# Kernel tuning notes

Hardware: AMD Instinct MI355X
Metric: run time of the kernel (lower is better)

Reference implementation:

```python
import jax, jax.numpy as jnp
import numpy as np

VOCAB = 50257
H = 512
T = 1024


def setup_inputs() -> dict:
    key = jax.random.key(0)
    k1, k2, k3, k4 = jax.random.split(key, 4)
    return {
        "tokens": jax.random.randint(k1, (T,), 0, VOCAB),
        "h0": jnp.zeros((H,), jnp.float32),
        "input_hidden": jax.random.normal(k2, (VOCAB, H), jnp.float32) * 0.01,
        "hidden_hidden": jax.random.normal(k3, (H, H), jnp.float32) * 0.01,
        "bias_hidden": jnp.zeros((H,), jnp.float32),
        "combined_weight": jax.random.normal(k4, (2 * H, VOCAB), jnp.float32) * 0.01,
        "bias_output": jnp.zeros((VOCAB,), jnp.float32),
    }


def reference(tokens, h0, input_hidden, hidden_hidden, bias_hidden,
              combined_weight, bias_output):
    T_ = tokens.shape[0]
    pos = jnp.arange(T_)
    emb = input_hidden[tokens]  # one-hot @ input_hidden == row gather, [T, H]

    def step(carry, xt):
        h, hist = carry              # h: [H], hist: [T, H] (rows >= t are zero)
        e, t = xt
        h = jnp.tanh(e + h @ hidden_hidden + bias_hidden)          # RNN cell
        scores = hist @ h                                          # [T]
        valid = pos < t                                            # causal mask over cache
        w = jax.nn.softmax(jnp.where(valid, scores, -1e30))
        ctx = jnp.where(t > 0, w @ hist, jnp.zeros_like(h))        # empty cache -> zeros
        out = jnp.concatenate([h, ctx]) @ combined_weight + bias_output
        hist = hist.at[t].set(h)
        return (h, hist), out

    init = (h0, jnp.zeros((T_, h0.shape[0]), h0.dtype))
    _, outs = jax.lax.scan(step, init, (emb, pos))
    return outs  # [T, VOCAB]
```

## Files before the change

kernel.cpp:

```cpp
#include <hip/hip_runtime.h>

typedef __attribute__((ext_vector_type(4))) float f32x4;
typedef __attribute__((ext_vector_type(8))) short short8;
typedef unsigned long long u64;

#define VOCAB 50257
#define HDIM 512
#define TLEN 1024
#define RNN_WGS 16
#define NANBITS 0x7fc00000u

#define GLOBAL_AS __attribute__((address_space(1)))
#define LDS_AS __attribute__((address_space(3)))
#define ASYNC16(gsrc, ldst) \
  __builtin_amdgcn_global_load_lds((const GLOBAL_AS void*)(gsrc), (LDS_AS void*)(ldst), 16, 0, 0)

static __device__ __forceinline__ unsigned short f2bf(float f) {
  unsigned u = __float_as_uint(f);
  u += 0x7fffu + ((u >> 16) & 1u);
  return (unsigned short)(u >> 16);
}
static __device__ __forceinline__ float b2f(short s) {
  return __uint_as_float(((unsigned)(unsigned short)s) << 16);
}

__global__ __launch_bounds__(256) void init_kernel(float* __restrict__ Hall) {
  int i = blockIdx.x * 256 + threadIdx.x;
  f32x4 v = {__uint_as_float(NANBITS), __uint_as_float(NANBITS),
             __uint_as_float(NANBITS), __uint_as_float(NANBITS)};
  ((f32x4*)Hall)[i] = v;
}

__global__ __launch_bounds__(256) void rnn_kernel(
    const int* __restrict__ tokens, const float* __restrict__ h0,
    const float* __restrict__ emb_table, const float* __restrict__ Whh,
    const float* __restrict__ bh, float* __restrict__ Hout)
{
  const int g = blockIdx.x;
  const int tid = threadIdx.x;
  const int col = tid & 31;
  const int kk = tid >> 5;
  const int colg = g * 32 + col;
  const int wvw = kk >> 1;
  const int kkl = kk & 1;

  __shared__ short8 Wl[2048];
  __shared__ float hl[HDIM];
  __shared__ float pl[256];

  unsigned short* Wls = (unsigned short*)Wl;
  for (int k = kk; k < HDIM; k += 8) {
    float w = Whh[k * HDIM + colg];
    int chunk = ((k >> 7) * 8 + ((k >> 3) & 7)) * 64 + ((k >> 6) & 1) * 32 + col;
    Wls[chunk * 8 + (k & 7)] = f2bf(w);
  }
  hl[tid] = h0[tid];
  hl[tid + 256] = h0[tid + 256];

  float e = 0.f;
  if (tid < 32) e = emb_table[(size_t)tokens[0] * HDIM + colg] + bh[colg];
  __syncthreads();

  for (int t = 0; t < TLEN; ++t) {
    float acc = 0.f;
#pragma unroll
    for (int i = 0; i < 8; ++i) {
      short8 w8 = Wl[(wvw * 8 + i) * 64 + kkl * 32 + col];
      f32x4 h1 = *(const f32x4*)&hl[kk * 64 + i * 8];
      f32x4 h2 = *(const f32x4*)&hl[kk * 64 + i * 8 + 4];
      acc += b2f(w8[0]) * h1.x + b2f(w8[1]) * h1.y + b2f(w8[2]) * h1.z + b2f(w8[3]) * h1.w
           + b2f(w8[4]) * h2.x + b2f(w8[5]) * h2.y + b2f(w8[6]) * h2.z + b2f(w8[7]) * h2.w;
    }
    pl[tid] = acc;
    __syncthreads();
    if (tid < 32) {
      float z = e;
#pragma unroll
      for (int q = 0; q < 8; ++q) z += pl[q * 32 + col];
      float h = tanhf(z);
      __hip_atomic_store(&Hout[t * HDIM + colg], h, __ATOMIC_RELAXED,
                         __HIP_MEMORY_SCOPE_AGENT);
      if (t + 1 < TLEN)
        e = emb_table[(size_t)tokens[t + 1] * HDIM + colg] + bh[colg];
    }
    if (t < TLEN - 1) {
      const u64* p = (const u64*)(Hout + t * HDIM) + tid;
      u64 v;
      do {
        v = __hip_atomic_load(p, __ATOMIC_RELAXED, __HIP_MEMORY_SCOPE_AGENT);
      } while (((unsigned)v == NANBITS) || ((unsigned)(v >> 32) == NANBITS));
      *(u64*)&hl[2 * tid] = v;
    }
    __syncthreads();
  }
}

__global__ __launch_bounds__(256) void attn_kernel(
    const float* __restrict__ Hall, unsigned short* __restrict__ Xbf)
{
  const int t = blockIdx.x;
  const int tid = threadIdx.x;
  const int lane = tid & 63;
  const int wave = tid >> 6;
  __shared__ float ht[HDIM];
  __shared__ float sc[TLEN];
  __shared__ float red[8];

  float h_a = Hall[(size_t)t * HDIM + tid];
  float h_b = Hall[(size_t)t * HDIM + tid + 256];
  ht[tid] = h_a; ht[tid + 256] = h_b;
  Xbf[(size_t)t * 1024 + tid] = f2bf(h_a);
  Xbf[(size_t)t * 1024 + tid + 256] = f2bf(h_b);
  __syncthreads();

  if (t == 0) {
    Xbf[512 + tid] = 0;
    Xbf[512 + tid + 256] = 0;
    return;
  }

  const f32x4* ht4 = (const f32x4*)ht;
  float lmax = -1e30f;
  for (int s = tid; s < t; s += 256) {
    const f32x4* hp = (const f32x4*)(Hall + (size_t)s * HDIM);
    float d = 0.f;
#pragma unroll 8
    for (int q = 0; q < HDIM / 4; ++q) {
      f32x4 a = hp[q]; f32x4 b = ht4[q];
      d += a.x * b.x + a.y * b.y + a.z * b.z + a.w * b.w;
    }
    sc[s] = d;
    lmax = fmaxf(lmax, d);
  }
  for (int off = 32; off > 0; off >>= 1) lmax = fmaxf(lmax, __shfl_down(lmax, off));
  if (lane == 0) red[wave] = lmax;
  __syncthreads();
  float m = fmaxf(fmaxf(red[0], red[1]), fmaxf(red[2], red[3]));
  __syncthreads();

  float lsum = 0.f;
  for (int s = tid; s < t; s += 256) {
    float ev = __expf(sc[s] - m);
    sc[s] = ev;
    lsum += ev;
  }
  for (int off = 32; off > 0; off >>= 1) lsum += __shfl_down(lsum, off);
  if (lane == 0) red[wave] = lsum;
  __syncthreads();
  float Z = red[0] + red[1] + red[2] + red[3];
  float inv = 1.0f / Z;

  float a0 = 0.f, a1 = 0.f;
#pragma unroll 4
  for (int s = 0; s < t; ++s) {
    float w = sc[s];
    a0 += w * Hall[(size_t)s * HDIM + tid];
    a1 += w * Hall[(size_t)s * HDIM + tid + 256];
  }
  Xbf[(size_t)t * 1024 + 512 + tid] = f2bf(a0 * inv);
  Xbf[(size_t)t * 1024 + 512 + tid + 256] = f2bf(a1 * inv);
}

__global__ __launch_bounds__(256) void convT_kernel(
    const float* __restrict__ Wc, unsigned short* __restrict__ WT)
{
  const int n0 = blockIdx.x * 64;
  const int k0 = blockIdx.y * 64;
  const int tid = threadIdx.x;
  __shared__ float tile[64][65];
  const int c = tid & 63;
  const int r = tid >> 6;
#pragma unroll
  for (int it = 0; it < 16; ++it) {
    int row = it * 4 + r;
    int n = n0 + c;
    tile[row][c] = (n < VOCAB) ? Wc[(size_t)(k0 + row) * VOCAB + n] : 0.f;
  }
  __syncthreads();
#pragma unroll
  for (int it = 0; it < 16; ++it) {
    int nr = it * 4 + r;
    int n = n0 + nr;
    if (n < VOCAB) WT[(size_t)n * 1024 + k0 + c] = f2bf(tile[c][nr]);
  }
}

__global__ __launch_bounds__(256) void gemm_kernel(
    const unsigned short* __restrict__ Xbf, const unsigned short* __restrict__ WT,
    const float* __restrict__ bias, float* __restrict__ out)
{
  const int n0 = blockIdx.x * 128;
  const int m0 = blockIdx.y * 128;
  const int tid = threadIdx.x;
  const int lane = tid & 63;
  const int wave = tid >> 6;
  const int wm = wave >> 1, wn = wave & 1;
  const int r15 = lane & 15, kq = lane >> 4;

  __shared__ short As[128 * 64];
  __shared__ short Bs[128 * 64];

  f32x4 acc[4][4] = {};

  for (int kb = 0; kb < 16; ++kb) {
#pragma unroll
    for (int j = 0; j < 4; ++j) {
      int slot = tid + 256 * j;
      int kc = slot >> 7, row = slot & 127;
      ASYNC16(Xbf + (size_t)(m0 + row) * 1024 + kb * 64 + kc * 8, As + slot * 8);
      int n = n0 + row; n = (n < VOCAB) ? n : (VOCAB - 1);
      ASYNC16(WT + (size_t)n * 1024 + kb * 64 + kc * 8, Bs + slot * 8);
    }
    __syncthreads();
#pragma unroll
    for (int s = 0; s < 2; ++s) {
      short8 af[4], bfr[4];
#pragma unroll
      for (int i = 0; i < 4; ++i)
        af[i] = *(const short8*)&As[(((s * 4 + kq) << 7) + wm * 64 + i * 16 + r15) * 8];
#pragma unroll
      for (int i = 0; i < 4; ++i)
        bfr[i] = *(const short8*)&Bs[(((s * 4 + kq) << 7) + wn * 64 + i * 16 + r15) * 8];
#pragma unroll
      for (int i = 0; i < 4; ++i)
#pragma unroll
        for (int jn = 0; jn < 4; ++jn)
          acc[i][jn] = __builtin_amdgcn_mfma_f32_16x16x32_bf16(af[i], bfr[jn], acc[i][jn], 0, 0, 0);
    }
    __syncthreads();
  }
#pragma unroll
  for (int i = 0; i < 4; ++i) {
    int row = m0 + wm * 64 + i * 16 + kq * 4;
#pragma unroll
    for (int jn = 0; jn < 4; ++jn) {
      int col = n0 + wn * 64 + jn * 16 + r15;
      if (col < VOCAB) {
        float bv = bias[col];
#pragma unroll
        for (int rr = 0; rr < 4; ++rr)
          out[(size_t)(row + rr) * VOCAB + col] = acc[i][jn][rr] + bv;
      }
    }
  }
}

extern "C" void kernel_launch(void* const* d_in, const int* in_sizes, int n_in,
                              void* d_out, int out_size, void* d_ws, size_t ws_size,
                              hipStream_t stream) {
  const int*   tokens   = (const int*)d_in[0];
  const float* h0       = (const float*)d_in[1];
  const float* emb      = (const float*)d_in[2];
  const float* Whh      = (const float*)d_in[3];
  const float* bh       = (const float*)d_in[4];
  const float* Wc       = (const float*)d_in[5];
  const float* bo       = (const float*)d_in[6];
  float* out = (float*)d_out;

  char* ws = (char*)d_ws;
  unsigned short* WT   = (unsigned short*)(ws);
  float*          Hall = (float*)(ws + 102926336);
  unsigned short* Xbf  = (unsigned short*)(ws + 105023488);

  init_kernel<<<dim3(512), dim3(256), 0, stream>>>(Hall);
  rnn_kernel<<<dim3(RNN_WGS), dim3(256), 0, stream>>>(tokens, h0, emb, Whh, bh, Hall);
  attn_kernel<<<dim3(TLEN), dim3(256), 0, stream>>>(Hall, Xbf);
  convT_kernel<<<dim3(786, 16), dim3(256), 0, stream>>>(Wc, WT);
  gemm_kernel<<<dim3(393, 8), dim3(256), 0, stream>>>(Xbf, WT, bo, out);
}
```

Before: 2.514 ms.

## Run RNN recurrence in a single workgroup using MFMA with register-resident weights

Replaces the 16-workgroup RNN, which synchronised every step through global-memory NaN-polling, with a single 512-thread workgroup. The recurrent weights are held as bf16 mostly in registers plus part in LDS, and each step's matrix-vector product runs as MFMA with only row 0 of the A operand non-zero. The hidden state is double-buffered in LDS as bf16, and the NaN-initialisation kernel is removed. This trades cross-workgroup global spin latency for a single CU doing all the compute, with higher register pressure and the hidden state now rounded to bf16 between steps.

```diff
diff --git a/kernel.cpp b/kernel.cpp
--- a/kernel.cpp
+++ b/kernel.cpp
@@ -2,97 +2,113 @@
 
 typedef __attribute__((ext_vector_type(4))) float f32x4;
 typedef __attribute__((ext_vector_type(8))) short short8;
-typedef unsigned long long u64;
 
 #define VOCAB 50257
 #define HDIM 512
 #define TLEN 1024
-#define RNN_WGS 16
-#define NANBITS 0x7fc00000u
-
-#define GLOBAL_AS __attribute__((address_space(1)))
-#define LDS_AS __attribute__((address_space(3)))
-#define ASYNC16(gsrc, ldst) \
-  __builtin_amdgcn_global_load_lds((const GLOBAL_AS void*)(gsrc), (LDS_AS void*)(ldst), 16, 0, 0)
 
 static __device__ __forceinline__ unsigned short f2bf(float f) {
   unsigned u = __float_as_uint(f);
   u += 0x7fffu + ((u >> 16) & 1u);
   return (unsigned short)(u >> 16);
 }
-static __device__ __forceinline__ float b2f(short s) {
-  return __uint_as_float(((unsigned)(unsigned short)s) << 16);
-}
-
-__global__ __launch_bounds__(256) void init_kernel(float* __restrict__ Hall) {
-  int i = blockIdx.x * 256 + threadIdx.x;
-  f32x4 v = {__uint_as_float(NANBITS), __uint_as_float(NANBITS),
-             __uint_as_float(NANBITS), __uint_as_float(NANBITS)};
-  ((f32x4*)Hall)[i] = v;
-}
-
-__global__ __launch_bounds__(256) void rnn_kernel(
+
+__global__ __launch_bounds__(512, 2) void rnn_kernel(
     const int* __restrict__ tokens, const float* __restrict__ h0,
     const float* __restrict__ emb_table, const float* __restrict__ Whh,
     const float* __restrict__ bh, float* __restrict__ Hout)
 {
-  const int g = blockIdx.x;
-  const int tid = threadIdx.x;
-  const int col = tid & 31;
-  const int kk = tid >> 5;
-  const int colg = g * 32 + col;
-  const int wvw = kk >> 1;
-  const int kkl = kk & 1;
-
-  __shared__ short8 Wl[2048];
-  __shared__ float hl[HDIM];
-  __shared__ float pl[256];
-
-  unsigned short* Wls = (unsigned short*)Wl;
-  for (int k = kk; k < HDIM; k += 8) {
-    float w = Whh[k * HDIM + colg];
-    int chunk = ((k >> 7) * 8 + ((k >> 3) & 7)) * 64 + ((k >> 6) & 1) * 32 + col;
-    Wls[chunk * 8 + (k & 7)] = f2bf(w);
-  }
-  hl[tid] = h0[tid];
-  hl[tid + 256] = h0[tid + 256];
-
-  float e = 0.f;
-  if (tid < 32) e = emb_table[(size_t)tokens[0] * HDIM + colg] + bh[colg];
-  __syncthreads();
-
-  for (int t = 0; t < TLEN; ++t) {
-    float acc = 0.f;
-#pragma unroll
-    for (int i = 0; i < 8; ++i) {
-      short8 w8 = Wl[(wvw * 8 + i) * 64 + kkl * 32 + col];
-      f32x4 h1 = *(const f32x4*)&hl[kk * 64 + i * 8];
-      f32x4 h2 = *(const f32x4*)&hl[kk * 64 + i * 8 + 4];
-      acc += b2f(w8[0]) * h1.x + b2f(w8[1]) * h1.y + b2f(w8[2]) * h1.z + b2f(w8[3]) * h1.w
-           + b2f(w8[4]) * h2.x + b2f(w8[5]) * h2.y + b2f(w8[6]) * h2.z + b2f(w8[7]) * h2.w;
-    }
-    pl[tid] = acc;
-    __syncthreads();
-    if (tid < 32) {
-      float z = e;
-#pragma unroll
-      for (int q = 0; q < 8; ++q) z += pl[q * 32 + col];
-      float h = tanhf(z);
-      __hip_atomic_store(&Hout[t * HDIM + colg], h, __ATOMIC_RELAXED,
-                         __HIP_MEMORY_SCOPE_AGENT);
-      if (t + 1 < TLEN)
-        e = emb_table[(size_t)tokens[t + 1] * HDIM + colg] + bh[colg];
-    }
-    if (t < TLEN - 1) {
-      const u64* p = (const u64*)(Hout + t * HDIM) + tid;
-      u64 v;
-      do {
-        v = __hip_atomic_load(p, __ATOMIC_RELAXED, __HIP_MEMORY_SCOPE_AGENT);
-      } while (((unsigned)v == NANBITS) || ((unsigned)(v >> 32) == NANBITS));
-      *(u64*)&hl[2 * tid] = v;
-    }
-    __syncthreads();
-  }
+  __shared__ short8 Wsp[8 * 16 * 64];
+  __shared__ __attribute__((aligned(16))) unsigned short hbuf[2][HDIM];
+  __shared__ int tokl[TLEN];
+
+  const int tid = threadIdx.x;
+  const int lane = tid & 63;
+  const int w = tid >> 6;
+  const int g = lane >> 4;
+  const int r = lane & 15;
+
+  short8 wf[4][12];
+#pragma unroll
+  for (int tl = 0; tl < 4; ++tl) {
+    const int col = w * 64 + tl * 16 + r;
+#pragma unroll
+    for (int kc = 0; kc < 16; ++kc) {
+      const int kb = kc * 32 + g * 8;
+      short8 v;
+#pragma unroll
+      for (int j = 0; j < 8; ++j)
+        v[j] = (short)f2bf(Whh[(size_t)(kb + j) * HDIM + col]);
+      if (kc < 12) wf[tl][kc] = v;
+      else         Wsp[(w * 16 + (kc - 12) * 4 + tl) * 64 + lane] = v;
+    }
+  }
+
+  if (tid < 256) {
+    unsigned pp = (unsigned)f2bf(h0[2 * tid]) | ((unsigned)f2bf(h0[2 * tid + 1]) << 16);
+    *(unsigned*)&hbuf[0][2 * tid] = pp;
+  }
+  tokl[tid] = tokens[tid];
+  tokl[tid + 512] = tokens[tid + 512];
+
+  float bhv[4] = {0.f, 0.f, 0.f, 0.f};
+  float e[4]   = {0.f, 0.f, 0.f, 0.f};
+  if (g == 0) {
+#pragma unroll
+    for (int tl = 0; tl < 4; ++tl) bhv[tl] = bh[w * 64 + tl * 16 + r];
+  }
+  __syncthreads();
+  {
+    int tok0 = tokl[0];
+    if (g == 0) {
+#pragma unroll
+      for (int tl = 0; tl < 4; ++tl)
+        e[tl] = emb_table[(size_t)tok0 * HDIM + w * 64 + tl * 16 + r] + bhv[tl];
+    }
+  }
+
+#define RNN_STEP(T, PS, PD)                                                       \
+  {                                                                               \
+    f32x4 acc[4] = {{0.f,0.f,0.f,0.f},{0.f,0.f,0.f,0.f},                          \
+                    {0.f,0.f,0.f,0.f},{0.f,0.f,0.f,0.f}};                         \
+    const unsigned short* hb = hbuf[PS];                                          \
+    short8 a = {};                                                                \
+    _Pragma("unroll")                                                             \
+    for (int kcp = 0; kcp < 4; ++kcp) {                                           \
+      if (r == 0) a = *(const short8*)(hb + (12 + kcp) * 32 + g * 8);             \
+      _Pragma("unroll")                                                           \
+      for (int tl = 0; tl < 4; ++tl) {                                            \
+        short8 b = Wsp[(w * 16 + kcp * 4 + tl) * 64 + lane];                      \
+        acc[tl] = __builtin_amdgcn_mfma_f32_16x16x32_bf16(a, b, acc[tl], 0, 0, 0);\
+      }                                                                           \
+    }                                                                             \
+    _Pragma("unroll")                                                             \
+    for (int kc = 0; kc < 12; ++kc) {                                             \
+      if (r == 0) a = *(const short8*)(hb + kc * 32 + g * 8);                     \
+      _Pragma("unroll")                                                           \
+      for (int tl = 0; tl < 4; ++tl)                                              \
+        acc[tl] = __builtin_amdgcn_mfma_f32_16x16x32_bf16(a, wf[tl][kc],          \
+                                                          acc[tl], 0, 0, 0);     \
+    }                                                                             \
+    if (g == 0) {                                                                 \
+      int tokn = tokl[((T) + 1) & (TLEN - 1)];                                    \
+      _Pragma("unroll")                                                           \
+      for (int tl = 0; tl < 4; ++tl) {                                            \
+        const int col = w * 64 + tl * 16 + r;                                     \
+        float hv = tanhf(acc[tl][0] + e[tl]);                                     \
+        Hout[(size_t)(T) * HDIM + col] = hv;                                      \
+        hbuf[PD][col] = f2bf(hv);                                                 \
+        e[tl] = emb_table[(size_t)tokn * HDIM + col] + bhv[tl];     \
+      }                                                                           \
+    }                                                                             \
+    __syncthreads();                                                              \
+  }
+
+  for (int t = 0; t < TLEN; t += 2) {
+    RNN_STEP(t, 0, 1)
+    RNN_STEP(t + 1, 1, 0)
+  }
+#undef RNN_STEP
 }
 
 __global__ __launch_bounds__(256) void attn_kernel(
@@ -184,6 +200,11 @@
     if (n < VOCAB) WT[(size_t)n * 1024 + k0 + c] = f2bf(tile[c][nr]);
   }
 }
+
+#define GLOBAL_AS __attribute__((address_space(1)))
+#define LDS_AS __attribute__((address_space(3)))
+#define ASYNC16(gsrc, ldst) \
+  __builtin_amdgcn_global_load_lds((const GLOBAL_AS void*)(gsrc), (LDS_AS void*)(ldst), 16, 0, 0)
 
 __global__ __launch_bounds__(256) void gemm_kernel(
     const unsigned short* __restrict__ Xbf, const unsigned short* __restrict__ WT,
@@ -262,8 +283,7 @@
   float*          Hall = (float*)(ws + 102926336);
   unsigned short* Xbf  = (unsigned short*)(ws + 105023488);
 
-  init_kernel<<<dim3(512), dim3(256), 0, stream>>>(Hall);
-  rnn_kernel<<<dim3(RNN_WGS), dim3(256), 0, stream>>>(tokens, h0, emb, Whh, bh, Hall);
+  rnn_kernel<<<dim3(1), dim3(512), 0, stream>>>(tokens, h0, emb, Whh, bh, Hall);
   attn_kernel<<<dim3(TLEN), dim3(256), 0, stream>>>(Hall, Xbf);
   convT_kernel<<<dim3(786, 16), dim3(256), 0, stream>>>(Wc, WT);
   gemm_kernel<<<dim3(393, 8), dim3(256), 0, stream>>>(Xbf, WT, bo, out);
```

Result: slower. 2.792 ms (+11.1%).
